# Kernel tuning notes

Measured on AMD Instinct MI355X. Metric: run time of the kernel, lower is better.

Reference implementation:

```python
import jax, jax.numpy as jnp
import numpy as np

N_NODES = 100000
N_EDGES = 300000
D_IN = 256
D_OUT = 256
NEG_SLOPE = 0.2


def setup_inputs() -> dict:
    key = jax.random.key(0)
    ks = jax.random.split(key, 6)
    feat = jax.random.normal(ks[0], (N_NODES, D_IN), dtype=jnp.float32)
    # xavier-normal-ish init scale
    scale = (2.0 / (D_IN + D_OUT)) ** 0.5
    W_src = jax.random.normal(ks[1], (D_IN, D_OUT), dtype=jnp.float32) * scale
    b_src = jnp.zeros((D_OUT,), dtype=jnp.float32)
    W_dst = jax.random.normal(ks[2], (D_IN, D_OUT), dtype=jnp.float32) * scale
    b_dst = jnp.zeros((D_OUT,), dtype=jnp.float32)
    attn = jax.random.normal(ks[3], (D_OUT,), dtype=jnp.float32) * scale
    src = jax.random.randint(ks[4], (N_EDGES,), 0, N_NODES, dtype=jnp.int32)
    dst = jax.random.randint(ks[5], (N_EDGES,), 0, N_NODES, dtype=jnp.int32)
    return {"feat": feat, "W_src": W_src, "b_src": b_src,
            "W_dst": W_dst, "b_dst": b_dst, "attn": attn,
            "src": src, "dst": dst}


def reference(feat, W_src, b_src, W_dst, b_dst, attn, src, dst):
    N = feat.shape[0]
    # node projections (dense GEMMs)
    el = feat @ W_src + b_src          # [N, D_OUT]  (feat_src / 'el')
    er = feat @ W_dst + b_dst          # [N, D_OUT]  (feat_dst / 'er')
    # edge-wise u_add_v + LeakyReLU, then attention dot
    e = jax.nn.leaky_relu(el[src] + er[dst], NEG_SLOPE)  # [E, D_OUT]
    score = e @ attn                    # [E]  ((e*attn).sum(-1))
    # edge softmax segmented by destination node
    smax = jax.ops.segment_max(score, dst, num_segments=N)   # [N]
    ex = jnp.exp(score - smax[dst])                           # [E]
    ssum = jax.ops.segment_sum(ex, dst, num_segments=N)      # [N]
    a = ex / ssum[dst]                                        # [E]
    # weighted scatter-sum aggregation: u_mul_e('el','a') -> sum per dst
    out = jax.ops.segment_sum(el[src] * a[:, None], dst, num_segments=N)
    return out  # [N, D_OUT]
```

## Files before the change

kernel.cpp:

```cpp
#include <hip/hip_runtime.h>
#include <cstdint>
#include <cmath>

#define D 256
#define NEG 0.2f
#define BK 64
#define NT (D/BK)

typedef __attribute__((ext_vector_type(8))) __bf16 bf16x8;
typedef __attribute__((ext_vector_type(8))) unsigned short ushort8;
typedef __attribute__((ext_vector_type(4))) float f32x4;

__device__ __forceinline__ unsigned short f2bf(float f){
    unsigned u = __float_as_uint(f);
    return (unsigned short)((u + 0x7fffu + ((u >> 16) & 1u)) >> 16);
}
__device__ __forceinline__ float b2f(unsigned short u){
    return __uint_as_float(((unsigned)u) << 16);
}

__device__ __forceinline__ void gload_lds16(const void* g, void* l){
    __builtin_amdgcn_global_load_lds(
        (const __attribute__((address_space(1))) unsigned int*)g,
        (__attribute__((address_space(3))) unsigned int*)l, 16, 0, 0);
}

__global__ __launch_bounds__(256) void prep_all_kernel(
    const float* __restrict__ Wsrc, const float* __restrict__ Wdst,
    const float* __restrict__ bsrc, const float* __restrict__ bdst,
    unsigned short* __restrict__ WT, float* __restrict__ biascat,
    const float* __restrict__ feat, unsigned short* __restrict__ featb,
    int N, int NPAD,
    const int* __restrict__ dst, int* __restrict__ deg, int E, int CB)
{
    const int b = blockIdx.x;
    if (b < 64) {
        int idx = b*256 + threadIdx.x;
        int col = idx >> 5;
        int u   = idx & 31;
        int gu  = (u & 24) | ((u ^ col) & 7);
        const float* W = (col < 256) ? Wsrc : Wdst;
        int c = col & 255;
        ushort8 o;
        #pragma unroll
        for (int j = 0; j < 8; ++j)
            o[j] = f2bf(W[(size_t)(gu*8 + j)*D + c]);
        *(ushort8*)(WT + (size_t)col*D + u*8) = o;
        if (idx < 512) biascat[idx] = (idx < 256) ? bsrc[idx] : bdst[idx-256];
    } else if (b < 64 + CB) {
        int e = (b - 64)*256 + threadIdx.x;
        if (e < E) atomicAdd(&deg[dst[e]], 1);
    } else {
        int nfb   = gridDim.x - 64 - CB;
        int total = NPAD * 32;
        for (int idx = (b - 64 - CB)*256 + threadIdx.x; idx < total; idx += nfb*256){
            int r = idx >> 5;
            int u = idx & 31;
            ushort8 o;
            if (r < N){
                int gu = (u & 24) | ((u ^ r) & 7);
                const float* s = feat + (size_t)r*D + gu*8;
                float4 a = *(const float4*)s;
                float4 bb = *(const float4*)(s + 4);
                o[0]=f2bf(a.x); o[1]=f2bf(a.y); o[2]=f2bf(a.z); o[3]=f2bf(a.w);
                o[4]=f2bf(bb.x); o[5]=f2bf(bb.y); o[6]=f2bf(bb.z); o[7]=f2bf(bb.w);
            } else {
                #pragma unroll
                for (int j = 0; j < 8; ++j) o[j] = 0;
            }
            *(ushort8*)(featb + (size_t)r*D + u*8) = o;
        }
    }
}

__global__ __launch_bounds__(256) void proj_mfma_kernel(
    const unsigned short* __restrict__ featb, const unsigned short* __restrict__ WT,
    const float* __restrict__ biascat,
    unsigned short* __restrict__ el16, unsigned short* __restrict__ er16, int N)
{
    __shared__ unsigned short As[2][128*BK];
    __shared__ unsigned short Bs[2][128*BK];

    const int b    = blockIdx.x;
    const int xcd  = b & 7;
    const int s    = b >> 3;
    const int p    = (s >> 2)*8 + xcd;
    const int c    = s & 3;
    const int row0 = p * 128;
    const int col0 = c * 128;

    const int tid  = threadIdx.x;
    const int wave = tid >> 6;
    const int lane = tid & 63;
    const int wr = (wave >> 1) * 64;
    const int wc = (wave & 1) * 64;
    const int l15 = lane & 15;
    const int kg  = lane >> 4;

    const int sr = (wave << 3) + (lane >> 3);
    const int sc = (lane & 7) * 8;

    f32x4 acc[4][4] = {};

    #pragma unroll
    for (int r4 = 0; r4 < 4; ++r4) {
        int ar = r4*32 + sr;
        gload_lds16(featb + (size_t)(row0 + ar)*D + 0 + sc, &As[0][(r4*32 + wave*8)*BK]);
        gload_lds16(WT    + (size_t)(col0 + ar)*D + 0 + sc, &Bs[0][(r4*32 + wave*8)*BK]);
    }

    for (int t = 0; t < NT; ++t) {
        const int cur = t & 1;
        if (t + 1 < NT) {
            int k0 = (t + 1) * BK;
            #pragma unroll
            for (int r4 = 0; r4 < 4; ++r4) {
                int ar = r4*32 + sr;
                gload_lds16(featb + (size_t)(row0 + ar)*D + k0 + sc,
                            &As[cur ^ 1][(r4*32 + wave*8)*BK]);
                gload_lds16(WT    + (size_t)(col0 + ar)*D + k0 + sc,
                            &Bs[cur ^ 1][(r4*32 + wave*8)*BK]);
            }
            asm volatile("s_waitcnt vmcnt(8)" ::: "memory");
        } else {
            asm volatile("s_waitcnt vmcnt(0)" ::: "memory");
        }
        __builtin_amdgcn_s_barrier();
        __builtin_amdgcn_sched_barrier(0);

        #pragma unroll
        for (int ks = 0; ks < 2; ++ks) {
            bf16x8 af[4], bfr[4];
            #pragma unroll
            for (int m = 0; m < 4; ++m){
                int row = wr + m*16 + l15;
                int cc = ((kg + ks*4) ^ (row & 7)) * 8;
                af[m] = *(const bf16x8*)&As[cur][row*BK + cc];
            }
            #pragma unroll
            for (int n = 0; n < 4; ++n){
                int row = wc + n*16 + l15;
                int cc = ((kg + ks*4) ^ (row & 7)) * 8;
                bfr[n] = *(const bf16x8*)&Bs[cur][row*BK + cc];
            }
            #pragma unroll
            for (int m = 0; m < 4; ++m)
                #pragma unroll
                for (int n = 0; n < 4; ++n)
                    acc[m][n] = __builtin_amdgcn_mfma_f32_16x16x32_bf16(bfr[n], af[m], acc[m][n], 0, 0, 0);
        }
        __builtin_amdgcn_sched_barrier(0);
        __builtin_amdgcn_s_barrier();
    }

    unsigned short* __restrict__ dstp = (col0 < 256) ? el16 : er16;
    const int ccbase = col0 & 255;
    #pragma unroll
    for (int m = 0; m < 4; ++m) {
        int row = row0 + wr + m*16 + l15;
        if (row >= N) continue;
        #pragma unroll
        for (int n = 0; n < 4; ++n) {
            int cw = wc + n*16 + kg*4;
            float4 b4 = *(const float4*)(biascat + col0 + cw);
            ushort4 o;
            o.x = f2bf(acc[m][n][0] + b4.x);
            o.y = f2bf(acc[m][n][1] + b4.y);
            o.z = f2bf(acc[m][n][2] + b4.z);
            o.w = f2bf(acc[m][n][3] + b4.w);
            *(ushort4*)(dstp + (size_t)row*D + ccbase + cw) = o;
        }
    }
}

__global__ __launch_bounds__(256) void scan_atomic_kernel(
    const int* __restrict__ deg, int* __restrict__ counter,
    int* __restrict__ rowstart, int* __restrict__ cursor, int N)
{
    int i    = blockIdx.x*256 + threadIdx.x;
    int lane = threadIdx.x & 63;
    int v = (i < N) ? deg[i] : 0;
    int pref = v;
    #pragma unroll
    for (int off = 1; off < 64; off <<= 1){
        int t = __shfl_up(pref, off, 64);
        if (lane >= off) pref += t;
    }
    int wtotal = __shfl(pref, 63, 64);
    int base = 0;
    if (lane == 63) base = atomicAdd(counter, wtotal);
    base = __shfl(base, 63, 64);
    if (i < N){
        int st = base + pref - v;
        rowstart[i] = st;
        cursor[i]   = st;
    }
}

__global__ void scatter_kernel(const int* __restrict__ dst, const int* __restrict__ src,
                               int* __restrict__ cursor, int* __restrict__ srcs, int E){
    int e = blockIdx.x*blockDim.x + threadIdx.x;
    if (e < E){
        int pos = atomicAdd(&cursor[dst[e]], 1);
        srcs[pos] = src[e];
    }
}

__global__ __launch_bounds__(256) void gat_node_kernel(
    const unsigned short* __restrict__ el16, const unsigned short* __restrict__ er16,
    const float* __restrict__ attn, const int* __restrict__ srcs,
    const int* __restrict__ rowstart, const int* __restrict__ degv,
    float* __restrict__ out, int N)
{
    int node = blockIdx.x*4 + (threadIdx.x >> 6);
    if (node >= N) return;
    int lane = threadIdx.x & 63;
    float4 o = make_float4(0.f,0.f,0.f,0.f);
    int deg = degv[node];
    float* op = out + (size_t)node*D + lane*4;
    if (deg == 0){ *(float4*)op = o; return; }

    ushort4 rv = *(const ushort4*)(er16 + (size_t)node*D + lane*4);
    float4 r4 = make_float4(b2f(rv.x), b2f(rv.y), b2f(rv.z), b2f(rv.w));
    float4 a4 = *(const float4*)(attn + lane*4);
    int start = rowstart[node];

    float m = -INFINITY, ssum = 0.f;
    for (int base = 0; base < deg; base += 4){
        int cnt = deg - base; if (cnt > 4) cnt = 4;
        float4 l[4]; float p[4];
        #pragma unroll
        for (int j = 0; j < 4; ++j){
            int k = base + j; if (k >= deg) k = deg - 1;
            int sn = srcs[start + k];
            ushort4 lv = *(const ushort4*)(el16 + (size_t)sn*D + lane*4);
            l[j] = make_float4(b2f(lv.x), b2f(lv.y), b2f(lv.z), b2f(lv.w));
        }
        #pragma unroll
        for (int j = 0; j < 4; ++j){
            float x, pp = 0.f;
            x = l[j].x + r4.x; pp += (x > 0.f ? x : NEG*x) * a4.x;
            x = l[j].y + r4.y; pp += (x > 0.f ? x : NEG*x) * a4.y;
            x = l[j].z + r4.z; pp += (x > 0.f ? x : NEG*x) * a4.z;
            x = l[j].w + r4.w; pp += (x > 0.f ? x : NEG*x) * a4.w;
            p[j] = pp;
        }
        #pragma unroll
        for (int off = 32; off > 0; off >>= 1){
            #pragma unroll
            for (int j = 0; j < 4; ++j) p[j] += __shfl_xor(p[j], off, 64);
        }
        #pragma unroll
        for (int j = 0; j < 4; ++j){
            if (j >= cnt) break;
            float newm  = fmaxf(m, p[j]);
            float scale = __expf(m - newm);
            float w     = __expf(p[j] - newm);
            ssum = ssum*scale + w;
            o.x = o.x*scale + w*l[j].x;
            o.y = o.y*scale + w*l[j].y;
            o.z = o.z*scale + w*l[j].z;
            o.w = o.w*scale + w*l[j].w;
            m = newm;
        }
    }
    float inv = 1.f/ssum;
    o.x *= inv; o.y *= inv; o.z *= inv; o.w *= inv;
    *(float4*)op = o;
}

extern "C" void kernel_launch(void* const* d_in, const int* in_sizes, int n_in,
                              void* d_out, int out_size, void* d_ws, size_t ws_size,
                              hipStream_t stream)
{
    const float* feat = (const float*)d_in[0];
    const float* Wsrc = (const float*)d_in[1];
    const float* bsrc = (const float*)d_in[2];
    const float* Wdst = (const float*)d_in[3];
    const float* bdst = (const float*)d_in[4];
    const float* attn = (const float*)d_in[5];
    const int*   src  = (const int*)d_in[6];
    const int*   dst  = (const int*)d_in[7];
    const int N = in_sizes[0] / D;
    const int E = in_sizes[6];
    const int NPAD = ((N + 1023)/1024)*1024;
    const int NP = NPAD / 128;
    float* out = (float*)d_out;

    unsigned short* el16 = (unsigned short*)d_ws;
    unsigned short* er16 = el16 + (size_t)N*D;
    int* deg      = (int*)(er16 + (size_t)N*D);
    int* counter  = deg + N;
    int* rowstart = counter + 4;
    int* cursor   = rowstart + N;
    int* srcs     = cursor + N;
    unsigned short* WT = (unsigned short*)(srcs + E);
    float* biascat = (float*)(WT + (size_t)512*D);
    unsigned short* featb = (unsigned short*)(biascat + 512);

    const int nb = (N + 255)/256;
    const int CB = (E + 255)/256;

    hipMemsetAsync(deg, 0, ((size_t)N + 4)*sizeof(int), stream);

    prep_all_kernel<<<64 + CB + 4096, 256, 0, stream>>>(
        Wsrc, Wdst, bsrc, bdst, WT, biascat, feat, featb, N, NPAD, dst, deg, E, CB);

    proj_mfma_kernel<<<4*NP, 256, 0, stream>>>(featb, WT, biascat, el16, er16, N);

    scan_atomic_kernel<<<nb, 256, 0, stream>>>(deg, counter, rowstart, cursor, N);
    scatter_kernel<<<(E + 255)/256, 256, 0, stream>>>(dst, src, cursor, srcs, E);

    gat_node_kernel<<<(N + 3)/4, 256, 0, stream>>>(el16, er16, attn, srcs,
                                                   rowstart, deg, out, N);
}
```

Measured before the change: 199.7 us.

## Remap feature-convert and node-aggregation blocks to match XCD-local panel ownership

The bf16 feature conversion and the per-node GAT aggregation now assign 128-row panels to blocks using the same XCD-interleaved mapping as the projection GEMM. Each panel is then produced and consumed on the same XCD. The goal is to keep featb and er16 rows in that XCD's L2 between kernels instead of refetching them from HBM or another die. The cost is extra index arithmetic, and it assumes NP is a multiple of 8 and that blocks are dispatched round-robin across XCDs.

Result: no change. 197.1 us (-1.3%).

```diff
diff --git a/kernel.cpp b/kernel.cpp
--- a/kernel.cpp
+++ b/kernel.cpp
@@ -30,7 +30,7 @@
     const float* __restrict__ bsrc, const float* __restrict__ bdst,
     unsigned short* __restrict__ WT, float* __restrict__ biascat,
     const float* __restrict__ feat, unsigned short* __restrict__ featb,
-    int N, int NPAD,
+    int N, int NP,
     const int* __restrict__ dst, int* __restrict__ deg, int E, int CB)
 {
     const int b = blockIdx.x;
@@ -51,11 +51,18 @@
         int e = (b - 64)*256 + threadIdx.x;
         if (e < E) atomicAdd(&deg[dst[e]], 1);
     } else {
-        int nfb   = gridDim.x - 64 - CB;
-        int total = NPAD * 32;
-        for (int idx = (b - 64 - CB)*256 + threadIdx.x; idx < total; idx += nfb*256){
-            int r = idx >> 5;
-            int u = idx & 31;
+        int f    = b - 64 - CB;
+        int nfb  = gridDim.x - 64 - CB;
+        int xcd  = f & 7;
+        int j    = f >> 3;
+        int perXCD = (NP/8) * 4096;
+        int stride = (nfb >> 3) * 256;
+        for (int idx = j*256 + threadIdx.x; idx < perXCD; idx += stride){
+            int plocal = idx >> 12;
+            int p      = plocal*8 + xcd;
+            int uin    = idx & 4095;
+            int r      = p*128 + (uin >> 5);
+            int u      = uin & 31;
             ushort8 o;
             if (r < N){
                 int gu = (u & 24) | ((u ^ r) & 7);
@@ -66,7 +73,7 @@
                 o[4]=f2bf(bb.x); o[5]=f2bf(bb.y); o[6]=f2bf(bb.z); o[7]=f2bf(bb.w);
             } else {
                 #pragma unroll
-                for (int j = 0; j < 8; ++j) o[j] = 0;
+                for (int jj = 0; jj < 8; ++jj) o[jj] = 0;
             }
             *(ushort8*)(featb + (size_t)r*D + u*8) = o;
         }
@@ -212,7 +219,11 @@
     const int* __restrict__ rowstart, const int* __restrict__ degv,
     float* __restrict__ out, int N)
 {
-    int node = blockIdx.x*4 + (threadIdx.x >> 6);
+    const int q   = blockIdx.x;
+    const int xcd = q & 7;
+    const int j   = q >> 3;
+    const int p   = (j >> 5)*8 + xcd;
+    int node = p*128 + (j & 31)*4 + (threadIdx.x >> 6);
     if (node >= N) return;
     int lane = threadIdx.x & 63;
     float4 o = make_float4(0.f,0.f,0.f,0.f);
@@ -228,39 +239,39 @@
     float m = -INFINITY, ssum = 0.f;
     for (int base = 0; base < deg; base += 4){
         int cnt = deg - base; if (cnt > 4) cnt = 4;
-        float4 l[4]; float p[4];
-        #pragma unroll
-        for (int j = 0; j < 4; ++j){
-            int k = base + j; if (k >= deg) k = deg - 1;
+        float4 l[4]; float pr[4];
+        #pragma unroll
+        for (int jj = 0; jj < 4; ++jj){
+            int k = base + jj; if (k >= deg) k = deg - 1;
             int sn = srcs[start + k];
             ushort4 lv = *(const ushort4*)(el16 + (size_t)sn*D + lane*4);
-            l[j] = make_float4(b2f(lv.x), b2f(lv.y), b2f(lv.z), b2f(lv.w));
-        }
-        #pragma unroll
-        for (int j = 0; j < 4; ++j){
+            l[jj] = make_float4(b2f(lv.x), b2f(lv.y), b2f(lv.z), b2f(lv.w));
+        }
+        #pragma unroll
+        for (int jj = 0; jj < 4; ++jj){
             float x, pp = 0.f;
-            x = l[j].x + r4.x; pp += (x > 0.f ? x : NEG*x) * a4.x;
-            x = l[j].y + r4.y; pp += (x > 0.f ? x : NEG*x) * a4.y;
-            x = l[j].z + r4.z; pp += (x > 0.f ? x : NEG*x) * a4.z;
-            x = l[j].w + r4.w; pp += (x > 0.f ? x : NEG*x) * a4.w;
-            p[j] = pp;
+            x = l[jj].x + r4.x; pp += (x > 0.f ? x : NEG*x) * a4.x;
+            x = l[jj].y + r4.y; pp += (x > 0.f ? x : NEG*x) * a4.y;
+            x = l[jj].z + r4.z; pp += (x > 0.f ? x : NEG*x) * a4.z;
+            x = l[jj].w + r4.w; pp += (x > 0.f ? x : NEG*x) * a4.w;
+            pr[jj] = pp;
         }
         #pragma unroll
         for (int off = 32; off > 0; off >>= 1){
             #pragma unroll
-            for (int j = 0; j < 4; ++j) p[j] += __shfl_xor(p[j], off, 64);
-        }
-        #pragma unroll
-        for (int j = 0; j < 4; ++j){
-            if (j >= cnt) break;
-            float newm  = fmaxf(m, p[j]);
+            for (int jj = 0; jj < 4; ++jj) pr[jj] += __shfl_xor(pr[jj], off, 64);
+        }
+        #pragma unroll
+        for (int jj = 0; jj < 4; ++jj){
+            if (jj >= cnt) break;
+            float newm  = fmaxf(m, pr[jj]);
             float scale = __expf(m - newm);
-            float w     = __expf(p[j] - newm);
+            float w     = __expf(pr[jj] - newm);
             ssum = ssum*scale + w;
-            o.x = o.x*scale + w*l[j].x;
-            o.y = o.y*scale + w*l[j].y;
-            o.z = o.z*scale + w*l[j].z;
-            o.w = o.w*scale + w*l[j].w;
+            o.x = o.x*scale + w*l[jj].x;
+            o.y = o.y*scale + w*l[jj].y;
+            o.z = o.z*scale + w*l[jj].z;
+            o.w = o.w*scale + w*l[jj].w;
             m = newm;
         }
     }
@@ -304,13 +315,13 @@
     hipMemsetAsync(deg, 0, ((size_t)N + 4)*sizeof(int), stream);
 
     prep_all_kernel<<<64 + CB + 4096, 256, 0, stream>>>(
-        Wsrc, Wdst, bsrc, bdst, WT, biascat, feat, featb, N, NPAD, dst, deg, E, CB);
+        Wsrc, Wdst, bsrc, bdst, WT, biascat, feat, featb, N, NP, dst, deg, E, CB);
 
     proj_mfma_kernel<<<4*NP, 256, 0, stream>>>(featb, WT, biascat, el16, er16, N);
 
     scan_atomic_kernel<<<nb, 256, 0, stream>>>(deg, counter, rowstart, cursor, N);
     scatter_kernel<<<(E + 255)/256, 256, 0, stream>>>(dst, src, cursor, srcs, E);
 
-    gat_node_kernel<<<(N + 3)/4, 256, 0, stream>>>(el16, er16, attn, srcs,
-                                                   rowstart, deg, out, N);
-}
+    gat_node_kernel<<<NP*32, 256, 0, stream>>>(el16, er16, attn, srcs,
+                                               rowstart, deg, out, N);
+}
```
